# Kernel tuning notes

Hardware: AMD Instinct MI355X
Metric: run time of the kernel (lower is better)

## Reference

```python
import jax, jax.numpy as jnp
import numpy as np

N = 50000   # nodes
E = 800000  # edges
H = 64      # hidden channels
EPS = 1e-16  # PyG softmax denominator epsilon


def _ptconv(x, pos, src, dst, W_src, W_dst, W_val, W_pos, b_pos):
    """PyG PointTransformerConv: per-edge gather, positional MLP, vector
    attention (segment softmax over edges grouped by dst), scatter-sum.
    edge_index convention: src = j (neighbor), dst = i (center)."""
    a_src = x @ W_src          # [N,H] alpha_j projection
    a_dst = x @ W_dst          # [N,H] alpha_i projection
    v = x @ W_val              # [N,H] values
    # relative positional encoding: pos_nn(pos_i - pos_j), [E,H]
    delta = (pos[dst] - pos[src]) @ W_pos + b_pos
    alpha = a_dst[dst] - a_src[src] + delta           # [E,H]
    # numerically-stable vector softmax over variable-size neighborhoods
    m = jax.lax.stop_gradient(jax.ops.segment_max(alpha, dst, num_segments=N))
    e = jnp.exp(alpha - m[dst])
    s = jax.ops.segment_sum(e, dst, num_segments=N)
    attn = e / (s[dst] + EPS)                         # [E,H]
    return jax.ops.segment_sum(attn * (v[src] + delta), dst, num_segments=N)


def setup_inputs() -> dict:
    key = jax.random.key(0)
    ks = jax.random.split(key, 16)
    x = jax.random.normal(ks[0], (N, 3), dtype=jnp.float32)
    pos = jax.random.normal(ks[1], (N, 3), dtype=jnp.float32)
    edge_index = jax.random.randint(ks[2], (2, E), 0, N)
    batch = jnp.zeros((N,), dtype=jnp.int32)

    def lin(k, i, o):
        return (jax.random.normal(k, (i, o), dtype=jnp.float32)
                * np.float32(1.0 / np.sqrt(i)))

    return {
        "x": x, "pos": pos, "edge_index": edge_index, "batch": batch,
        # conv1 (in=3 -> H)
        "W1_src": lin(ks[3], 3, H), "W1_dst": lin(ks[4], 3, H),
        "W1_val": lin(ks[5], 3, H),
        "W1_pos": lin(ks[6], 3, H), "b1_pos": jnp.zeros((H,), jnp.float32),
        # conv2 (H -> H)
        "W2_src": lin(ks[7], H, H), "W2_dst": lin(ks[8], H, H),
        "W2_val": lin(ks[9], H, H),
        "W2_pos": lin(ks[10], 3, H), "b2_pos": jnp.zeros((H,), jnp.float32),
        # MLP head
        "W_fc1": lin(ks[11], H, H // 2), "b_fc1": jnp.zeros((H // 2,), jnp.float32),
        "W_fc2": lin(ks[12], H // 2, 1), "b_fc2": jnp.zeros((1,), jnp.float32),
    }


def reference(x, pos, edge_index, batch,
              W1_src, W1_dst, W1_val, W1_pos, b1_pos,
              W2_src, W2_dst, W2_val, W2_pos, b2_pos,
              W_fc1, b_fc1, W_fc2, b_fc2):
    src, dst = edge_index[0], edge_index[1]
    h = jax.nn.relu(_ptconv(x, pos, src, dst, W1_src, W1_dst, W1_val, W1_pos, b1_pos))
    h = jax.nn.relu(_ptconv(h, pos, src, dst, W2_src, W2_dst, W2_val, W2_pos, b2_pos))
    h = jax.nn.relu(h @ W_fc1 + b_fc1)
    return h @ W_fc2 + b_fc2  # [N, 1]
```

## Files before the change

kernel.cpp:

```cpp
#include <hip/hip_runtime.h>
#include <hip/hip_fp16.h>
#include <math.h>


#define LOG2E 1.44269504088896340736f

typedef _Float16 hf2 __attribute__((ext_vector_type(2)));
union H2U { __half2 hh; hf2 hf; unsigned u; };

#if defined(__has_builtin)
#if __has_builtin(__builtin_amdgcn_fdot2)
#define HAVE_FDOT2 1
#endif
#endif

__device__ __forceinline__ float fdot2(hf2 a, hf2 b, float c) {
#ifdef HAVE_FDOT2
    return __builtin_amdgcn_fdot2(a, b, c, false);
#else
    return fmaf((float)a.x, (float)b.x, fmaf((float)a.y, (float)b.y, c));
#endif
}

__device__ __forceinline__ unsigned bf16_rn(float x) {
    unsigned b = __float_as_uint(x);
    return (b + 0x7FFFu + ((b >> 16) & 1u)) >> 16;
}

__device__ __forceinline__ unsigned pack_payload(float a_plus_c, float vv) {
    float t = fminf(fmaxf(-a_plus_c * LOG2E, -86.0f), 86.0f);
    float E = exp2f(t);
    return (bf16_rn(E) << 16) | bf16_rn(E * vv);
}

__global__ void __launch_bounds__(256) hist_proj1_kernel(
        const int* __restrict__ dst, int* __restrict__ count, int* __restrict__ rank,
        const float* __restrict__ x, const float* __restrict__ pos,
        const float* __restrict__ W1_src, const float* __restrict__ W1_val,
        const float* __restrict__ W1_pos,
        unsigned* __restrict__ g1, int N, int E) {
    int gtid = blockIdx.x * 256 + threadIdx.x;
    int gsz = gridDim.x * 256;
    for (int e = gtid; e < E; e += gsz)
        rank[e] = atomicAdd(&count[dst[e]], 1);

    int lane = threadIdx.x & 63, wid = threadIdx.x >> 6;
    float ws0 = W1_src[lane], ws1 = W1_src[64 + lane], ws2 = W1_src[128 + lane];
    float wv0 = W1_val[lane], wv1 = W1_val[64 + lane], wv2 = W1_val[128 + lane];
    float wp0 = W1_pos[lane], wp1 = W1_pos[64 + lane], wp2 = W1_pos[128 + lane];
    int nwav = gridDim.x * 4;
    for (int node = blockIdx.x * 4 + wid; node < N; node += nwav) {
        float x0 = x[node * 3 + 0], x1 = x[node * 3 + 1], x2 = x[node * 3 + 2];
        float p0 = pos[node * 3 + 0], p1 = pos[node * 3 + 1], p2 = pos[node * 3 + 2];
        float as = fmaf(x0, ws0, fmaf(x1, ws1, x2 * ws2));
        float vv = fmaf(x0, wv0, fmaf(x1, wv1, x2 * wv2));
        float cc = fmaf(p0, wp0, fmaf(p1, wp1, p2 * wp2));
        g1[node * 64 + lane] = pack_payload(as + cc, vv - cc);
    }
}

__global__ void __launch_bounds__(256) scan_kernel(
        const int* __restrict__ count, int* __restrict__ offsets, int n, int nsb) {
    __shared__ int red[4];
    __shared__ int wpre[4];
    int tid = threadIdx.x, lane = tid & 63, wid = tid >> 6;
    int lim = blockIdx.x * 1024;
    int s = 0;
    for (int i = tid * 4; i < lim; i += 1024) {
        int4 c = *(const int4*)&count[i];
        s += c.x + c.y + c.z + c.w;
    }
    #pragma unroll
    for (int off = 32; off >= 1; off >>= 1) s += __shfl_down(s, off);
    if (lane == 0) red[wid] = s;
    __syncthreads();
    int base = red[0] + red[1] + red[2] + red[3];

    int b4 = lim + tid * 4;
    int4 c = make_int4(0, 0, 0, 0);
    if (b4 + 3 < n) {
        c = *(const int4*)&count[b4];
    } else {
        if (b4 + 0 < n) c.x = count[b4 + 0];
        if (b4 + 1 < n) c.y = count[b4 + 1];
        if (b4 + 2 < n) c.z = count[b4 + 2];
    }
    int tsum = c.x + c.y + c.z + c.w;
    int inc = tsum;
    #pragma unroll
    for (int off = 1; off < 64; off <<= 1) {
        int t2 = __shfl_up(inc, off);
        if (lane >= off) inc += t2;
    }
    if (lane == 63) wpre[wid] = inc;
    __syncthreads();
    int wbase = 0;
    for (int q = 0; q < wid; ++q) wbase += wpre[q];
    int excl = base + wbase + (inc - tsum);
    if (b4 + 0 < n) offsets[b4 + 0] = excl;
    if (b4 + 1 < n) offsets[b4 + 1] = excl + c.x;
    if (b4 + 2 < n) offsets[b4 + 2] = excl + c.x + c.y;
    if (b4 + 3 < n) offsets[b4 + 3] = excl + c.x + c.y + c.z;
    if ((int)blockIdx.x == nsb - 1 && tid == 0)
        offsets[n] = base + wpre[0] + wpre[1] + wpre[2] + wpre[3];
}

__global__ void __launch_bounds__(256) scatter_kernel(
        const int* __restrict__ src, const int* __restrict__ dst,
        const int* __restrict__ rank, const int* __restrict__ offsets,
        int* __restrict__ sorted_src, int E) {
    int e = blockIdx.x * 256 + threadIdx.x;
    if (e < E) sorted_src[offsets[dst[e]] + rank[e]] = src[e];
}

__device__ __forceinline__ void eacc(unsigned u, float& s, float& n) {
    s += __uint_as_float(u & 0xFFFF0000u);
    n += __uint_as_float(u << 16);
}

__device__ __forceinline__ float edge_node(
        int node, int laneoff,
        const int* __restrict__ offsets, const int* __restrict__ ss,
        const char* __restrict__ gbase, float dv) {
    int beg = offsets[node], end = offsets[node + 1];
    if (beg >= end) return 0.f;
    float s0 = 0.f, n0 = 0.f, s1 = 0.f, n1 = 0.f;
    int e = beg;
    int aligned = min((beg + 3) & ~3, end);
    for (; e < aligned; ++e) {
        int i0 = __builtin_amdgcn_readfirstlane(ss[e]);
        unsigned g0 = *(const unsigned*)(gbase + (((size_t)(unsigned)i0) << 8) + laneoff);
        eacc(g0, s0, n0);
    }
    for (; e + 8 <= end; e += 8) {
        int4 ia = *(const int4*)(ss + e);
        int4 ib = *(const int4*)(ss + e + 4);
        int i0 = __builtin_amdgcn_readfirstlane(ia.x);
        int i1 = __builtin_amdgcn_readfirstlane(ia.y);
        int i2 = __builtin_amdgcn_readfirstlane(ia.z);
        int i3 = __builtin_amdgcn_readfirstlane(ia.w);
        int i4 = __builtin_amdgcn_readfirstlane(ib.x);
        int i5 = __builtin_amdgcn_readfirstlane(ib.y);
        int i6 = __builtin_amdgcn_readfirstlane(ib.z);
        int i7 = __builtin_amdgcn_readfirstlane(ib.w);
        unsigned g0 = *(const unsigned*)(gbase + (((size_t)(unsigned)i0) << 8) + laneoff);
        unsigned g1 = *(const unsigned*)(gbase + (((size_t)(unsigned)i1) << 8) + laneoff);
        unsigned g2 = *(const unsigned*)(gbase + (((size_t)(unsigned)i2) << 8) + laneoff);
        unsigned g3 = *(const unsigned*)(gbase + (((size_t)(unsigned)i3) << 8) + laneoff);
        unsigned g4 = *(const unsigned*)(gbase + (((size_t)(unsigned)i4) << 8) + laneoff);
        unsigned g5 = *(const unsigned*)(gbase + (((size_t)(unsigned)i5) << 8) + laneoff);
        unsigned g6 = *(const unsigned*)(gbase + (((size_t)(unsigned)i6) << 8) + laneoff);
        unsigned g7 = *(const unsigned*)(gbase + (((size_t)(unsigned)i7) << 8) + laneoff);
        eacc(g0, s0, n0);
        eacc(g1, s1, n1);
        eacc(g2, s0, n0);
        eacc(g3, s1, n1);
        eacc(g4, s0, n0);
        eacc(g5, s1, n1);
        eacc(g6, s0, n0);
        eacc(g7, s1, n1);
    }
    for (; e + 4 <= end; e += 4) {
        int4 ia = *(const int4*)(ss + e);
        int i0 = __builtin_amdgcn_readfirstlane(ia.x);
        int i1 = __builtin_amdgcn_readfirstlane(ia.y);
        int i2 = __builtin_amdgcn_readfirstlane(ia.z);
        int i3 = __builtin_amdgcn_readfirstlane(ia.w);
        unsigned g0 = *(const unsigned*)(gbase + (((size_t)(unsigned)i0) << 8) + laneoff);
        unsigned g1 = *(const unsigned*)(gbase + (((size_t)(unsigned)i1) << 8) + laneoff);
        unsigned g2 = *(const unsigned*)(gbase + (((size_t)(unsigned)i2) << 8) + laneoff);
        unsigned g3 = *(const unsigned*)(gbase + (((size_t)(unsigned)i3) << 8) + laneoff);
        eacc(g0, s0, n0);
        eacc(g1, s1, n1);
        eacc(g2, s0, n0);
        eacc(g3, s1, n1);
    }
    for (; e < end; ++e) {
        int i0 = __builtin_amdgcn_readfirstlane(ss[e]);
        unsigned g0 = *(const unsigned*)(gbase + (((size_t)(unsigned)i0) << 8) + laneoff);
        eacc(g0, s0, n0);
    }
    float s = s0 + s1;
    float r = __builtin_amdgcn_rcpf(s + 1e-37f);
    return fmaxf(fmaf(n0 + n1, r, dv), 0.f);
}

__global__ void __launch_bounds__(256, 8) e1p2_kernel(
        const float* __restrict__ pos,
        const int* __restrict__ offsets, const int* __restrict__ sorted_src,
        const unsigned* __restrict__ g1,
        const float* __restrict__ W1_pos, const float* __restrict__ b1_pos,
        const float* __restrict__ W2_src, const float* __restrict__ W2_val,
        const float* __restrict__ W2_pos,
        unsigned* __restrict__ g2, int N) {
    __shared__ uint4 W4q[16 * 64];
    __shared__ __half hsh[4][64];
    int tid = threadIdx.x, lane = tid & 63, wid = tid >> 6;
    for (int idx = tid; idx < 1024; idx += 256) {
        int q = idx >> 6, c = idx & 63, k = 4 * q;
        H2U s01, s23, v01, v23;
        s01.hh = __floats2half2_rn(W2_src[k * 64 + c], W2_src[(k + 1) * 64 + c]);
        s23.hh = __floats2half2_rn(W2_src[(k + 2) * 64 + c], W2_src[(k + 3) * 64 + c]);
        v01.hh = __floats2half2_rn(W2_val[k * 64 + c], W2_val[(k + 1) * 64 + c]);
        v23.hh = __floats2half2_rn(W2_val[(k + 2) * 64 + c], W2_val[(k + 3) * 64 + c]);
        W4q[idx] = make_uint4(s01.u, s23.u, v01.u, v23.u);
    }
    __syncthreads();

    float w1p0 = W1_pos[lane], w1p1 = W1_pos[64 + lane], w1p2 = W1_pos[128 + lane];
    float bp1 = b1_pos[lane];
    float w2p0 = W2_pos[lane], w2p1 = W2_pos[64 + lane], w2p2 = W2_pos[128 + lane];
    int laneoff = lane * 4;
    int nwav = gridDim.x * 4;

    for (int node = blockIdx.x * 4 + wid; node < N; node += nwav) {
        float p0 = pos[node * 3 + 0], p1 = pos[node * 3 + 1], p2 = pos[node * 3 + 2];
        float dpos = fmaf(p0, w1p0, fmaf(p1, w1p1, p2 * w1p2));
        float hval = edge_node(node, laneoff, offsets, sorted_src,
                               (const char*)g1, dpos + bp1);
        hsh[wid][lane] = __float2half(hval);
        const uint2* hq = (const uint2*)hsh[wid];
        float as = 0.f, vv = 0.f;
        #pragma unroll 4
        for (int q = 0; q < 16; ++q) {
            uint2 hu = hq[q];
            H2U h01, h23; h01.u = hu.x; h23.u = hu.y;
            uint4 wq = W4q[q * 64 + lane];
            H2U a0, a1, b0, b1;
            a0.u = wq.x; a1.u = wq.y; b0.u = wq.z; b1.u = wq.w;
            as = fdot2(h01.hf, a0.hf, as);
            as = fdot2(h23.hf, a1.hf, as);
            vv = fdot2(h01.hf, b0.hf, vv);
            vv = fdot2(h23.hf, b1.hf, vv);
        }
        float cc = fmaf(p0, w2p0, fmaf(p1, w2p1, p2 * w2p2));
        g2[node * 64 + lane] = pack_payload(as + cc, vv - cc);
    }
}

__global__ void __launch_bounds__(256, 8) e2head_kernel(
        const float* __restrict__ pos,
        const int* __restrict__ offsets, const int* __restrict__ sorted_src,
        const unsigned* __restrict__ g2,
        const float* __restrict__ W2_pos, const float* __restrict__ b2_pos,
        const float* __restrict__ Wfc1, const float* __restrict__ bfc1,
        const float* __restrict__ Wfc2, const float* __restrict__ bfc2,
        float* __restrict__ out, int N) {
    __shared__ __half hsh[4][64];
    int tid = threadIdx.x, lane = tid & 63, wid = tid >> 6;
    int c = lane & 31, khb = (lane >> 5) * 16;
    unsigned Wr[16];
    #pragma unroll
    for (int j = 0; j < 16; ++j) {
        H2U w;
        w.hh = __floats2half2_rn(Wfc1[(2 * (khb + j)) * 32 + c],
                                 Wfc1[(2 * (khb + j) + 1) * 32 + c]);
        Wr[j] = w.u;
    }

    float wp0 = W2_pos[lane], wp1 = W2_pos[64 + lane], wp2 = W2_pos[128 + lane];
    float bp = b2_pos[lane];
    float bfc1c = bfc1[c], wfc2c = Wfc2[c], bias2 = bfc2[0];
    int laneoff = lane * 4;
    int nwav = gridDim.x * 4;

    for (int node = blockIdx.x * 4 + wid; node < N; node += nwav) {
        float p0 = pos[node * 3 + 0], p1 = pos[node * 3 + 1], p2 = pos[node * 3 + 2];
        float dpos = fmaf(p0, wp0, fmaf(p1, wp1, p2 * wp2));
        float hval = edge_node(node, laneoff, offsets, sorted_src,
                               (const char*)g2, dpos + bp);
        hsh[wid][lane] = __float2half(hval);
        const hf2* h2 = (const hf2*)hsh[wid];
        float t2 = 0.f;
        #pragma unroll
        for (int j = 0; j < 16; ++j) {
            hf2 hk = h2[khb + j];
            H2U w; w.u = Wr[j];
            t2 = fdot2(hk, w.hf, t2);
        }
        t2 += __shfl_down(t2, 32);
        t2 = fmaxf(t2 + bfc1c, 0.f) * wfc2c;
        t2 = (lane < 32) ? t2 : 0.f;
        #pragma unroll
        for (int off = 16; off >= 1; off >>= 1) t2 += __shfl_down(t2, off);
        if (lane == 0) out[node] = t2 + bias2;
    }
}

extern "C" void kernel_launch(void* const* d_in, const int* in_sizes, int n_in,
                              void* d_out, int out_size, void* d_ws, size_t ws_size,
                              hipStream_t stream) {
    const float* x   = (const float*)d_in[0];
    const float* pos = (const float*)d_in[1];
    const int* eidx  = (const int*)d_in[2];
    const float* W1_src = (const float*)d_in[4];
    const float* W1_val = (const float*)d_in[6];
    const float* W1_pos = (const float*)d_in[7];
    const float* b1_pos = (const float*)d_in[8];
    const float* W2_src = (const float*)d_in[9];
    const float* W2_val = (const float*)d_in[11];
    const float* W2_pos = (const float*)d_in[12];
    const float* b2_pos = (const float*)d_in[13];
    const float* W_fc1  = (const float*)d_in[14];
    const float* b_fc1  = (const float*)d_in[15];
    const float* W_fc2  = (const float*)d_in[16];
    const float* b_fc2  = (const float*)d_in[17];

    const int N = in_sizes[0] / 3;
    const int E = in_sizes[2] / 2;
    const int* src = eidx;
    const int* dst = eidx + E;
    const int nsb = (N + 1023) / 1024;

    char* w = (char*)d_ws;
    auto carve = [&](size_t bytes) -> void* {
        void* p = (void*)w;
        w += (bytes + 255) & ~size_t(255);
        return p;
    };
    int*      count      = (int*)carve((size_t)N * 4);
    int*      offsets    = (int*)carve((size_t)(N + 1) * 4);
    int*      rank       = (int*)carve((size_t)E * 4);
    int*      sorted_src = (int*)carve((size_t)E * 4);
    unsigned* g1         = (unsigned*)carve((size_t)N * 64 * 4);
    unsigned* g2         = (unsigned*)carve((size_t)N * 64 * 4);

    hipMemsetAsync(count, 0, (size_t)N * 4, stream);
    hist_proj1_kernel<<<2048, 256, 0, stream>>>(
        dst, count, rank, x, pos, W1_src, W1_val, W1_pos, g1, N, E);
    scan_kernel<<<nsb, 256, 0, stream>>>(count, offsets, N, nsb);
    scatter_kernel<<<(E + 255) / 256, 256, 0, stream>>>(src, dst, rank, offsets,
                                                        sorted_src, E);
    e1p2_kernel<<<2048, 256, 0, stream>>>(
        pos, offsets, sorted_src, g1, W1_pos, b1_pos, W2_src, W2_val, W2_pos, g2, N);
    e2head_kernel<<<2048, 256, 0, stream>>>(
        pos, offsets, sorted_src, g2, W2_pos, b2_pos,
        W_fc1, b_fc1, W_fc2, b_fc2, (float*)d_out, N);
}
```

Baseline: 231.5 us.

## Privatize destination histogram into eight replicas to cut atomic contention

The per-destination edge count atomics are spread across eight count arrays chosen by block index. The scan sums all replicas to build CSR offsets and also writes a per-replica base table. The scatter kernel uses the matching replica base plus each edge's rank, with the grid fixed at 2048 blocks so the block-to-replica mapping matches the histogram. This trades lower contention on the random atomics for an eightfold larger memset, extra scan reads and writes, and more scattered base lookups.

Result: slower. 258.3 us (+11.6%).

```diff
diff --git a/kernel.cpp b/kernel.cpp
--- a/kernel.cpp
+++ b/kernel.cpp
@@ -34,15 +34,16 @@
 }
 
 __global__ void __launch_bounds__(256) hist_proj1_kernel(
-        const int* __restrict__ dst, int* __restrict__ count, int* __restrict__ rank,
+        const int* __restrict__ dst, int* __restrict__ count8, int* __restrict__ rank,
         const float* __restrict__ x, const float* __restrict__ pos,
         const float* __restrict__ W1_src, const float* __restrict__ W1_val,
         const float* __restrict__ W1_pos,
         unsigned* __restrict__ g1, int N, int E) {
     int gtid = blockIdx.x * 256 + threadIdx.x;
     int gsz = gridDim.x * 256;
+    int* cnt = count8 + (blockIdx.x & 7) * N;
     for (int e = gtid; e < E; e += gsz)
-        rank[e] = atomicAdd(&count[dst[e]], 1);
+        rank[e] = atomicAdd(&cnt[dst[e]], 1);
 
     int lane = threadIdx.x & 63, wid = threadIdx.x >> 6;
     float ws0 = W1_src[lane], ws1 = W1_src[64 + lane], ws2 = W1_src[128 + lane];
@@ -60,15 +61,20 @@
 }
 
 __global__ void __launch_bounds__(256) scan_kernel(
-        const int* __restrict__ count, int* __restrict__ offsets, int n, int nsb) {
+        const int* __restrict__ count8, int* __restrict__ offsets,
+        int* __restrict__ base8, int n, int nsb) {
     __shared__ int red[4];
     __shared__ int wpre[4];
     int tid = threadIdx.x, lane = tid & 63, wid = tid >> 6;
     int lim = blockIdx.x * 1024;
     int s = 0;
-    for (int i = tid * 4; i < lim; i += 1024) {
-        int4 c = *(const int4*)&count[i];
-        s += c.x + c.y + c.z + c.w;
+    #pragma unroll
+    for (int j = 0; j < 8; ++j) {
+        const int* cj = count8 + j * n;
+        for (int i = tid * 4; i < lim; i += 1024) {
+            int4 c = *(const int4*)&cj[i];
+            s += c.x + c.y + c.z + c.w;
+        }
     }
     #pragma unroll
     for (int off = 32; off >= 1; off >>= 1) s += __shfl_down(s, off);
@@ -77,15 +83,27 @@
     int base = red[0] + red[1] + red[2] + red[3];
 
     int b4 = lim + tid * 4;
-    int4 c = make_int4(0, 0, 0, 0);
-    if (b4 + 3 < n) {
-        c = *(const int4*)&count[b4];
-    } else {
-        if (b4 + 0 < n) c.x = count[b4 + 0];
-        if (b4 + 1 < n) c.y = count[b4 + 1];
-        if (b4 + 2 < n) c.z = count[b4 + 2];
-    }
-    int tsum = c.x + c.y + c.z + c.w;
+    int c[8][4];
+    #pragma unroll
+    for (int j = 0; j < 8; ++j) {
+        int4 v = make_int4(0, 0, 0, 0);
+        if (b4 + 3 < n) {
+            v = *(const int4*)&count8[j * n + b4];
+        } else {
+            if (b4 + 0 < n) v.x = count8[j * n + b4 + 0];
+            if (b4 + 1 < n) v.y = count8[j * n + b4 + 1];
+            if (b4 + 2 < n) v.z = count8[j * n + b4 + 2];
+        }
+        c[j][0] = v.x; c[j][1] = v.y; c[j][2] = v.z; c[j][3] = v.w;
+    }
+    int tot[4];
+    #pragma unroll
+    for (int k = 0; k < 4; ++k) {
+        tot[k] = 0;
+        #pragma unroll
+        for (int j = 0; j < 8; ++j) tot[k] += c[j][k];
+    }
+    int tsum = tot[0] + tot[1] + tot[2] + tot[3];
     int inc = tsum;
     #pragma unroll
     for (int off = 1; off < 64; off <<= 1) {
@@ -96,21 +114,34 @@
     __syncthreads();
     int wbase = 0;
     for (int q = 0; q < wid; ++q) wbase += wpre[q];
-    int excl = base + wbase + (inc - tsum);
-    if (b4 + 0 < n) offsets[b4 + 0] = excl;
-    if (b4 + 1 < n) offsets[b4 + 1] = excl + c.x;
-    if (b4 + 2 < n) offsets[b4 + 2] = excl + c.x + c.y;
-    if (b4 + 3 < n) offsets[b4 + 3] = excl + c.x + c.y + c.z;
+    int run = base + wbase + (inc - tsum);
+    #pragma unroll
+    for (int k = 0; k < 4; ++k) {
+        int i = b4 + k;
+        if (i < n) {
+            offsets[i] = run;
+            int pb = run;
+            #pragma unroll
+            for (int j = 0; j < 8; ++j) {
+                base8[j * n + i] = pb;
+                pb += c[j][k];
+            }
+            run += tot[k];
+        }
+    }
     if ((int)blockIdx.x == nsb - 1 && tid == 0)
         offsets[n] = base + wpre[0] + wpre[1] + wpre[2] + wpre[3];
 }
 
 __global__ void __launch_bounds__(256) scatter_kernel(
         const int* __restrict__ src, const int* __restrict__ dst,
-        const int* __restrict__ rank, const int* __restrict__ offsets,
-        int* __restrict__ sorted_src, int E) {
-    int e = blockIdx.x * 256 + threadIdx.x;
-    if (e < E) sorted_src[offsets[dst[e]] + rank[e]] = src[e];
+        const int* __restrict__ rank, const int* __restrict__ base8,
+        int* __restrict__ sorted_src, int N, int E) {
+    int gtid = blockIdx.x * 256 + threadIdx.x;
+    int gsz = gridDim.x * 256;
+    const int* bj = base8 + (blockIdx.x & 7) * N;
+    for (int e = gtid; e < E; e += gsz)
+        sorted_src[bj[dst[e]] + rank[e]] = src[e];
 }
 
 __device__ __forceinline__ void eacc(unsigned u, float& s, float& n) {
@@ -318,19 +349,20 @@
         w += (bytes + 255) & ~size_t(255);
         return p;
     };
-    int*      count      = (int*)carve((size_t)N * 4);
+    int*      count8     = (int*)carve((size_t)8 * N * 4);
     int*      offsets    = (int*)carve((size_t)(N + 1) * 4);
+    int*      base8      = (int*)carve((size_t)8 * N * 4);
     int*      rank       = (int*)carve((size_t)E * 4);
     int*      sorted_src = (int*)carve((size_t)E * 4);
     unsigned* g1         = (unsigned*)carve((size_t)N * 64 * 4);
     unsigned* g2         = (unsigned*)carve((size_t)N * 64 * 4);
 
-    hipMemsetAsync(count, 0, (size_t)N * 4, stream);
+    hipMemsetAsync(count8, 0, (size_t)8 * N * 4, stream);
     hist_proj1_kernel<<<2048, 256, 0, stream>>>(
-        dst, count, rank, x, pos, W1_src, W1_val, W1_pos, g1, N, E);
-    scan_kernel<<<nsb, 256, 0, stream>>>(count, offsets, N, nsb);
-    scatter_kernel<<<(E + 255) / 256, 256, 0, stream>>>(src, dst, rank, offsets,
-                                                        sorted_src, E);
+        dst, count8, rank, x, pos, W1_src, W1_val, W1_pos, g1, N, E);
+    scan_kernel<<<nsb, 256, 0, stream>>>(count8, offsets, base8, N, nsb);
+    scatter_kernel<<<2048, 256, 0, stream>>>(src, dst, rank, base8,
+                                             sorted_src, N, E);
     e1p2_kernel<<<2048, 256, 0, stream>>>(
         pos, offsets, sorted_src, g1, W1_pos, b1_pos, W2_src, W2_val, W2_pos, g2, N);
     e2head_kernel<<<2048, 256, 0, stream>>>(
```
